# Performance work log

Measured on AMD Instinct MI355X. Metric: run time of the kernel, lower is better.

The kernel has to match this reference:

```python
import jax, jax.numpy as jnp
import numpy as np
import math

B, S, D = 2, 2048, 1024
H, KV, HD = 16, 4, 64
N_REP = H // KV
ROPE_THETA = 1.0e6


def _rope_tables(seq_len, head_dim, theta):
    inv_freq = 1.0 / (theta ** (np.arange(0, head_dim, 2, dtype=np.float32) / head_dim))
    t = np.arange(seq_len, dtype=np.float32)
    freqs = np.outer(t, inv_freq)                      # [S, HD/2]
    emb = np.concatenate([freqs, freqs], axis=-1)      # [S, HD]
    return jnp.asarray(np.cos(emb)), jnp.asarray(np.sin(emb))


def setup_inputs() -> dict:
    key = jax.random.key(0)
    ks = jax.random.split(key, 6)
    cos, sin = _rope_tables(S, HD, ROPE_THETA)
    scale = 0.02
    return {
        "x": jax.random.normal(ks[0], (B, S, D), dtype=jnp.float32),
        "cos": cos,
        "sin": sin,
        "Wq": jax.random.normal(ks[1], (D, H * HD), dtype=jnp.float32) * scale,
        "Wk": jax.random.normal(ks[2], (D, KV * HD), dtype=jnp.float32) * scale,
        "Wv": jax.random.normal(ks[3], (D, KV * HD), dtype=jnp.float32) * scale,
        "Wo": jax.random.normal(ks[4], (H * HD, D), dtype=jnp.float32) * scale,
    }


def _rotate_half(u):
    u1, u2 = u[..., : HD // 2], u[..., HD // 2 :]
    return jnp.concatenate([-u2, u1], axis=-1)


def reference(x, cos, sin, Wq, Wk, Wv, Wo):
    bsz, seq_len, _ = x.shape
    q = (x @ Wq).reshape(bsz, seq_len, H, HD)   # [B,S,H,HD]
    k = (x @ Wk).reshape(bsz, seq_len, KV, HD)  # [B,S,KV,HD]
    v = (x @ Wv).reshape(bsz, seq_len, KV, HD)

    # RoPE: cos/sin [S,HD] broadcast over batch and heads (unsqueeze_dim=1)
    c = cos[:seq_len][None, :, None, :]
    s = sin[:seq_len][None, :, None, :]
    q = q * c + _rotate_half(q) * s
    k = k * c + _rotate_half(k) * s

    # repeat_kv: expand KV heads groupwise to H heads
    k = jnp.repeat(k, N_REP, axis=2)  # [B,S,H,HD]
    v = jnp.repeat(v, N_REP, axis=2)

    q = q.transpose(0, 2, 1, 3)  # [B,H,S,HD]
    k = k.transpose(0, 2, 1, 3)
    v = v.transpose(0, 2, 1, 3)

    scores = jnp.einsum("bhqd,bhkd->bhqk", q, k) / math.sqrt(HD)
    causal = jnp.tril(jnp.ones((seq_len, seq_len), dtype=bool))
    scores = jnp.where(causal[None, None], scores, jnp.finfo(jnp.float32).min)
    probs = jax.nn.softmax(scores.astype(jnp.float32), axis=-1).astype(x.dtype)

    out = jnp.einsum("bhqk,bhkd->bhqd", probs, v)        # [B,H,S,HD]
    out = out.transpose(0, 2, 1, 3).reshape(bsz, seq_len, H * HD)
    return out @ Wo
```

## Files before the change

### kernel.cpp

```cpp
#include <hip/hip_runtime.h>

#define SS 2048
#define NH 16
#define NKV 4
#define HD 64

typedef __bf16 bf16;
typedef __bf16 bf16x8 __attribute__((ext_vector_type(8)));
typedef float f32x4 __attribute__((ext_vector_type(4)));

#define SM_SCALE 0.18033688011f

__device__ __forceinline__ void gl_lds16(const bf16* g, bf16* l) {
    __builtin_amdgcn_global_load_lds((const __attribute__((address_space(1))) void*)g,
                                     (__attribute__((address_space(3))) void*)l, 16, 0, 0);
}

__global__ __launch_bounds__(256) void prep_kernel(
    const float* __restrict__ Wq, const float* __restrict__ Wk,
    const float* __restrict__ Wv, const float* __restrict__ Wo,
    bf16* __restrict__ wqkv_t, bf16* __restrict__ wo_t)
{
    const int blk = blockIdx.x;
    const int tid = threadIdx.x;
    const float* W; bf16* Wt; int N, n0, k0;
    if (blk < 256)      { W = Wq; Wt = wqkv_t;                       N = 1024; n0 = (blk & 15) * 64;         k0 = (blk >> 4) * 64; }
    else if (blk < 320) { W = Wk; Wt = wqkv_t + (size_t)1024 * 1024; N = 256;  n0 = ((blk - 256) & 3) * 64;  k0 = ((blk - 256) >> 2) * 64; }
    else if (blk < 384) { W = Wv; Wt = wqkv_t + (size_t)1280 * 1024; N = 256;  n0 = ((blk - 320) & 3) * 64;  k0 = ((blk - 320) >> 2) * 64; }
    else                { W = Wo; Wt = wo_t;                         N = 1024; n0 = ((blk - 384) & 15) * 64; k0 = ((blk - 384) >> 4) * 64; }

    __shared__ float Ts[64][65];
    const int c = tid & 63, rr = tid >> 6;
    #pragma unroll
    for (int i = 0; i < 16; ++i) {
        const int kk = i * 4 + rr;
        Ts[kk][c] = W[(size_t)(k0 + kk) * N + n0 + c];
    }
    __syncthreads();
    #pragma unroll
    for (int i = 0; i < 16; ++i) {
        const int nn = i * 4 + rr;
        Wt[(size_t)(n0 + nn) * 1024 + k0 + c] = (bf16)Ts[c][nn];
    }
}

template<int EPI>
__global__ __launch_bounds__(256) void gemm_bt_kernel(
    const bf16* __restrict__ A, const float* __restrict__ Af,
    const bf16* __restrict__ Bt, float* __restrict__ C,
    const float* __restrict__ cosp, const float* __restrict__ sinp,
    bf16* __restrict__ qo, bf16* __restrict__ ko, bf16* __restrict__ vto,
    int M, int N, int K)
{
    __shared__ bf16 As[64 * 64];
    __shared__ bf16 Bs[128 * 64];
    const int m0 = blockIdx.x * 64, n0 = blockIdx.y * 128;
    const int tid = threadIdx.x;
    const int w = tid >> 6, lane = tid & 63, g = lane >> 4, li = lane & 15;
    const int wm = w >> 1, wn = w & 1;

    f32x4 acc[2][4];
    const f32x4 z = {0.f, 0.f, 0.f, 0.f};
    #pragma unroll
    for (int i = 0; i < 2; ++i)
        #pragma unroll
        for (int j = 0; j < 4; ++j) acc[i][j] = z;

    const int srow = tid >> 3;
    const int schunk = ((tid & 7) ^ (srow & 7)) * 8;
    const bf16* pB0 = Bt + (size_t)(n0 + srow) * K + schunk;
    const bf16* pB1 = Bt + (size_t)(n0 + 32 + srow) * K + schunk;
    const bf16* pB2 = Bt + (size_t)(n0 + 64 + srow) * K + schunk;
    const bf16* pB3 = Bt + (size_t)(n0 + 96 + srow) * K + schunk;
    bf16* lB0 = Bs + (size_t)w * 512;
    bf16* lB1 = Bs + 2048 + (size_t)w * 512;
    bf16* lB2 = Bs + 4096 + (size_t)w * 512;
    bf16* lB3 = Bs + 6144 + (size_t)w * 512;
    const bf16* pA0 = (EPI == 0) ? A + (size_t)(m0 + srow) * K + schunk : nullptr;
    const bf16* pA1 = (EPI == 0) ? A + (size_t)(m0 + 32 + srow) * K + schunk : nullptr;
    bf16* lA0 = As + (size_t)w * 512;
    bf16* lA1 = As + 2048 + (size_t)w * 512;

    for (int kk = 0; kk < K; kk += 64) {
        __syncthreads();
        if (EPI == 0) {
            gl_lds16(pA0 + kk, lA0);
            gl_lds16(pA1 + kk, lA1);
        } else {
            #pragma unroll
            for (int s = 0; s < 2; ++s) {
                const float* src = Af + (size_t)(m0 + s * 32 + srow) * K + kk + (tid & 7) * 8;
                const float4 v0 = *(const float4*)src;
                const float4 v1 = *(const float4*)(src + 4);
                bf16x8 t8;
                t8[0] = (bf16)v0.x; t8[1] = (bf16)v0.y; t8[2] = (bf16)v0.z; t8[3] = (bf16)v0.w;
                t8[4] = (bf16)v1.x; t8[5] = (bf16)v1.y; t8[6] = (bf16)v1.z; t8[7] = (bf16)v1.w;
                *(bf16x8*)&As[(s * 32 + srow) * 64 + schunk] = t8;
            }
        }
        gl_lds16(pB0 + kk, lB0);
        gl_lds16(pB1 + kk, lB1);
        gl_lds16(pB2 + kk, lB2);
        gl_lds16(pB3 + kk, lB3);
        __syncthreads();
        #pragma unroll
        for (int t = 0; t < 2; ++t) {
            const int phys = ((t * 4 + g) ^ (li & 7)) * 8;
            bf16x8 af[2], bfr[4];
            #pragma unroll
            for (int mi = 0; mi < 2; ++mi) af[mi] = *(const bf16x8*)&As[(wm * 32 + mi * 16 + li) * 64 + phys];
            #pragma unroll
            for (int ni = 0; ni < 4; ++ni) bfr[ni] = *(const bf16x8*)&Bs[(wn * 64 + ni * 16 + li) * 64 + phys];
            #pragma unroll
            for (int mi = 0; mi < 2; ++mi)
                #pragma unroll
                for (int ni = 0; ni < 4; ++ni)
                    acc[mi][ni] = __builtin_amdgcn_mfma_f32_16x16x32_bf16(af[mi], bfr[ni], acc[mi][ni], 0, 0, 0);
        }
    }

    const int row0 = m0 + wm * 32, col0 = n0 + wn * 64;
    if (EPI == 0) {
        #pragma unroll
        for (int mi = 0; mi < 2; ++mi)
            #pragma unroll
            for (int ni = 0; ni < 4; ++ni)
                #pragma unroll
                for (int r = 0; r < 4; ++r)
                    C[(size_t)(row0 + mi * 16 + g * 4 + r) * N + col0 + ni * 16 + li] = acc[mi][ni][r];
    } else {
        #pragma unroll
        for (int ni = 0; ni < 4; ++ni) {
            const int col = col0 + ni * 16 + li;
            const int d = col & 63;
            #pragma unroll
            for (int mi = 0; mi < 2; ++mi) {
                #pragma unroll
                for (int r = 0; r < 4; ++r) {
                    const int row = row0 + mi * 16 + g * 4 + r;
                    const int bb = row >> 11, s = row & 2047;
                    float val = acc[mi][ni][r];
                    if (col < 1280) {
                        const float pairv = acc[mi][ni ^ 2][r];
                        const float rot = (d < 32) ? -pairv : pairv;
                        val = val * cosp[s * 64 + d] + rot * sinp[s * 64 + d];
                    }
                    if (col < 1024) {
                        const int hh = col >> 6;
                        qo[(((size_t)bb * NH + hh) * SS + s) * HD + d] = (bf16)(val * SM_SCALE);
                    } else if (col < 1280) {
                        const int kh = (col - 1024) >> 6;
                        ko[(((size_t)bb * NKV + kh) * SS + s) * HD + d] = (bf16)val;
                    } else {
                        const int kh = (col - 1280) >> 6;
                        vto[(((size_t)bb * NKV + kh) * HD + d) * SS + s] = (bf16)val;
                    }
                }
            }
        }
    }
}

__global__ __launch_bounds__(256) void flash_kernel(const bf16* __restrict__ q, const bf16* __restrict__ k,
                                                    const bf16* __restrict__ vt, bf16* __restrict__ o)
{
    __shared__ bf16 Ks[128 * 64];
    __shared__ bf16 Vt[64 * 128];
    __shared__ bf16 Ps[4][16][72];

    const int blk = blockIdx.x;
    const int qt = 31 - (blk >> 5);
    const int h = blk & 15;
    const int b = (blk >> 4) & 1;
    const int kvh = h >> 2;
    const int tid = threadIdx.x;
    const int w = tid >> 6, lane = tid & 63, g = lane >> 4, li = lane & 15;

    const bf16* qh = q + ((size_t)b * NH + h) * SS * HD;
    const bf16* kh = k + ((size_t)b * NKV + kvh) * SS * HD;
    const bf16* vh = vt + ((size_t)b * NKV + kvh) * (size_t)HD * SS;

    bf16x8 ones;
    #pragma unroll
    for (int j = 0; j < 8; ++j) ones[j] = (bf16)1.0f;
    const f32x4 z = {0.f, 0.f, 0.f, 0.f};

    const bf16* qrow = qh + (size_t)(qt * 64 + w * 16 + li) * HD;
    bf16x8 qf[2];
    qf[0] = *(const bf16x8*)(qrow + g * 8);
    qf[1] = *(const bf16x8*)(qrow + 32 + g * 8);

    const int ksrow = tid >> 3;
    const int kchunk = ((tid & 7) ^ (ksrow & 7)) * 8;
    const int vsrow = tid >> 4;
    const int vchunk = (((tid & 15) ^ (vsrow & 7)) & 15) * 8;
    bf16* lK = Ks + (size_t)w * 512;
    bf16* lV = Vt + (size_t)w * 512;

    f32x4 o_acc[4], l_acc;
    #pragma unroll
    for (int nt = 0; nt < 4; ++nt) o_acc[nt] = z;
    l_acc = z;

    for (int kt0 = 0; kt0 <= qt; kt0 += 2) {
        __syncthreads();
        {
            #pragma unroll
            for (int s = 0; s < 4; ++s)
                gl_lds16(kh + (size_t)(kt0 * 64 + s * 32 + ksrow) * HD + kchunk, lK + s * 2048);
            #pragma unroll
            for (int s = 0; s < 4; ++s)
                gl_lds16(vh + (size_t)(s * 16 + vsrow) * SS + kt0 * 64 + vchunk, lV + s * 2048);
        }
        __syncthreads();

        #pragma unroll
        for (int sub = 0; sub < 2; ++sub) {
            const int kt = kt0 + sub;
            if (kt > qt) break;

            f32x4 s_acc[4];
            #pragma unroll
            for (int nt = 0; nt < 4; ++nt) s_acc[nt] = z;
            #pragma unroll
            for (int t = 0; t < 2; ++t)
                #pragma unroll
                for (int nt = 0; nt < 4; ++nt) {
                    const bf16x8 kf = *(const bf16x8*)&Ks[(sub * 64 + nt * 16 + li) * 64 + (((t * 4 + g) ^ (li & 7)) * 8)];
                    s_acc[nt] = __builtin_amdgcn_mfma_f32_16x16x32_bf16(qf[t], kf, s_acc[nt], 0, 0, 0);
                }

            if (kt == qt) {
                const int qr0 = qt * 64 + w * 16 + g * 4;
                #pragma unroll
                for (int nt = 0; nt < 4; ++nt) {
                    const int key = kt * 64 + nt * 16 + li;
                    #pragma unroll
                    for (int r = 0; r < 4; ++r) {
                        float sv = s_acc[nt][r];
                        if (key > qr0 + r) sv = -1e30f;
                        Ps[w][g * 4 + r][(nt * 16 + li) ^ (g * 16)] = (bf16)exp2f(sv);
                    }
                }
            } else {
                #pragma unroll
                for (int nt = 0; nt < 4; ++nt)
                    #pragma unroll
                    for (int r = 0; r < 4; ++r)
                        Ps[w][g * 4 + r][(nt * 16 + li) ^ (g * 16)] = (bf16)exp2f(s_acc[nt][r]);
            }

            #pragma unroll
            for (int t = 0; t < 2; ++t) {
                const bf16x8 pf = *(const bf16x8*)&Ps[w][li][(t * 32 + g * 8) ^ ((li >> 2) * 16)];
                l_acc = __builtin_amdgcn_mfma_f32_16x16x32_bf16(pf, ones, l_acc, 0, 0, 0);
                #pragma unroll
                for (int nt = 0; nt < 4; ++nt) {
                    const bf16x8 vf = *(const bf16x8*)&Vt[(nt * 16 + li) * 128 + (((sub * 8 + t * 4 + g) ^ (li & 7)) * 8)];
                    o_acc[nt] = __builtin_amdgcn_mfma_f32_16x16x32_bf16(pf, vf, o_acc[nt], 0, 0, 0);
                }
            }
        }
    }

    #pragma unroll
    for (int r = 0; r < 4; ++r) {
        const float inv = 1.f / l_acc[r];
        const int s = qt * 64 + w * 16 + g * 4 + r;
        bf16* orow = o + (((size_t)b * SS + s) * NH + h) * HD;
        #pragma unroll
        for (int nt = 0; nt < 4; ++nt) orow[nt * 16 + li] = (bf16)(o_acc[nt][r] * inv);
    }
}

extern "C" void kernel_launch(void* const* d_in, const int* in_sizes, int n_in,
                              void* d_out, int out_size, void* d_ws, size_t ws_size,
                              hipStream_t stream) {
    const float* x     = (const float*)d_in[0];
    const float* cos_t = (const float*)d_in[1];
    const float* sin_t = (const float*)d_in[2];
    const float* Wq    = (const float*)d_in[3];
    const float* Wk    = (const float*)d_in[4];
    const float* Wv    = (const float*)d_in[5];
    const float* Wo    = (const float*)d_in[6];
    float* out = (float*)d_out;

    char* wsb = (char*)d_ws;
    bf16* o_b    = (bf16*)(wsb);
    bf16* wqkv_t = (bf16*)(wsb + 8388608);
    bf16* wo_t   = (bf16*)(wsb + 11534336);
    bf16* q_b    = (bf16*)(wsb + 13631488);
    bf16* k_b    = (bf16*)(wsb + 22020096);
    bf16* vt_b   = (bf16*)(wsb + 24117248);

    prep_kernel<<<640, 256, 0, stream>>>(Wq, Wk, Wv, Wo, wqkv_t, wo_t);

    gemm_bt_kernel<2><<<dim3(64, 12), 256, 0, stream>>>(nullptr, x, wqkv_t, nullptr, cos_t, sin_t,
                                                        q_b, k_b, vt_b, 4096, 1536, 1024);
    flash_kernel<<<1024, 256, 0, stream>>>(q_b, k_b, vt_b, o_b);
    gemm_bt_kernel<0><<<dim3(64, 8), 256, 0, stream>>>(o_b, nullptr, wo_t, out, nullptr, nullptr,
                                                       nullptr, nullptr, nullptr, 4096, 1024, 1024);
}
```

Baseline: 166.7 us.

## Enlarge GEMM M-tile to 128 and transpose QK^T MFMA for vectorized P stores

Both GEMMs now use 128x128 output tiles instead of 64x128, with each wave computing 64x64 and the grid halved in the M dimension. This raises operand reuse per LDS load but cuts block count to 384 and 256, which may underfill the GPU's CUs. In the flash kernel, the QK^T MFMA operands are swapped so each lane holds four consecutive keys for one query row. P is then written to LDS as bf16x4 vectors in an XOR-swizzled layout, replacing scalar stores, and the causal mask indexing is adjusted to match.

```diff
diff --git a/kernel.cpp b/kernel.cpp
--- a/kernel.cpp
+++ b/kernel.cpp
@@ -6,6 +6,7 @@
 #define HD 64
 
 typedef __bf16 bf16;
+typedef __bf16 bf16x4 __attribute__((ext_vector_type(4)));
 typedef __bf16 bf16x8 __attribute__((ext_vector_type(8)));
 typedef float f32x4 __attribute__((ext_vector_type(4)));
 
@@ -52,43 +53,42 @@
     bf16* __restrict__ qo, bf16* __restrict__ ko, bf16* __restrict__ vto,
     int M, int N, int K)
 {
-    __shared__ bf16 As[64 * 64];
+    __shared__ bf16 As[128 * 64];
     __shared__ bf16 Bs[128 * 64];
-    const int m0 = blockIdx.x * 64, n0 = blockIdx.y * 128;
+    const int m0 = blockIdx.x * 128, n0 = blockIdx.y * 128;
     const int tid = threadIdx.x;
     const int w = tid >> 6, lane = tid & 63, g = lane >> 4, li = lane & 15;
     const int wm = w >> 1, wn = w & 1;
 
-    f32x4 acc[2][4];
+    f32x4 acc[4][4];
     const f32x4 z = {0.f, 0.f, 0.f, 0.f};
     #pragma unroll
-    for (int i = 0; i < 2; ++i)
+    for (int i = 0; i < 4; ++i)
         #pragma unroll
         for (int j = 0; j < 4; ++j) acc[i][j] = z;
 
     const int srow = tid >> 3;
     const int schunk = ((tid & 7) ^ (srow & 7)) * 8;
-    const bf16* pB0 = Bt + (size_t)(n0 + srow) * K + schunk;
-    const bf16* pB1 = Bt + (size_t)(n0 + 32 + srow) * K + schunk;
-    const bf16* pB2 = Bt + (size_t)(n0 + 64 + srow) * K + schunk;
-    const bf16* pB3 = Bt + (size_t)(n0 + 96 + srow) * K + schunk;
-    bf16* lB0 = Bs + (size_t)w * 512;
-    bf16* lB1 = Bs + 2048 + (size_t)w * 512;
-    bf16* lB2 = Bs + 4096 + (size_t)w * 512;
-    bf16* lB3 = Bs + 6144 + (size_t)w * 512;
-    const bf16* pA0 = (EPI == 0) ? A + (size_t)(m0 + srow) * K + schunk : nullptr;
-    const bf16* pA1 = (EPI == 0) ? A + (size_t)(m0 + 32 + srow) * K + schunk : nullptr;
-    bf16* lA0 = As + (size_t)w * 512;
-    bf16* lA1 = As + 2048 + (size_t)w * 512;
+    const bf16* pB[4];
+    const bf16* pA[4];
+    bf16* lB[4];
+    bf16* lA[4];
+    #pragma unroll
+    for (int s = 0; s < 4; ++s) {
+        pB[s] = Bt + (size_t)(n0 + s * 32 + srow) * K + schunk;
+        lB[s] = Bs + s * 2048 + (size_t)w * 512;
+        if (EPI == 0) pA[s] = A + (size_t)(m0 + s * 32 + srow) * K + schunk;
+        lA[s] = As + s * 2048 + (size_t)w * 512;
+    }
 
     for (int kk = 0; kk < K; kk += 64) {
         __syncthreads();
         if (EPI == 0) {
-            gl_lds16(pA0 + kk, lA0);
-            gl_lds16(pA1 + kk, lA1);
+            #pragma unroll
+            for (int s = 0; s < 4; ++s) gl_lds16(pA[s] + kk, lA[s]);
         } else {
             #pragma unroll
-            for (int s = 0; s < 2; ++s) {
+            for (int s = 0; s < 4; ++s) {
                 const float* src = Af + (size_t)(m0 + s * 32 + srow) * K + kk + (tid & 7) * 8;
                 const float4 v0 = *(const float4*)src;
                 const float4 v1 = *(const float4*)(src + 4);
@@ -98,31 +98,29 @@
                 *(bf16x8*)&As[(s * 32 + srow) * 64 + schunk] = t8;
             }
         }
-        gl_lds16(pB0 + kk, lB0);
-        gl_lds16(pB1 + kk, lB1);
-        gl_lds16(pB2 + kk, lB2);
-        gl_lds16(pB3 + kk, lB3);
+        #pragma unroll
+        for (int s = 0; s < 4; ++s) gl_lds16(pB[s] + kk, lB[s]);
         __syncthreads();
         #pragma unroll
         for (int t = 0; t < 2; ++t) {
             const int phys = ((t * 4 + g) ^ (li & 7)) * 8;
-            bf16x8 af[2], bfr[4];
-            #pragma unroll
-            for (int mi = 0; mi < 2; ++mi) af[mi] = *(const bf16x8*)&As[(wm * 32 + mi * 16 + li) * 64 + phys];
+            bf16x8 af[4], bfr[4];
+            #pragma unroll
+            for (int mi = 0; mi < 4; ++mi) af[mi] = *(const bf16x8*)&As[(wm * 64 + mi * 16 + li) * 64 + phys];
             #pragma unroll
             for (int ni = 0; ni < 4; ++ni) bfr[ni] = *(const bf16x8*)&Bs[(wn * 64 + ni * 16 + li) * 64 + phys];
             #pragma unroll
-            for (int mi = 0; mi < 2; ++mi)
+            for (int mi = 0; mi < 4; ++mi)
                 #pragma unroll
                 for (int ni = 0; ni < 4; ++ni)
                     acc[mi][ni] = __builtin_amdgcn_mfma_f32_16x16x32_bf16(af[mi], bfr[ni], acc[mi][ni], 0, 0, 0);
         }
     }
 
-    const int row0 = m0 + wm * 32, col0 = n0 + wn * 64;
+    const int row0 = m0 + wm * 64, col0 = n0 + wn * 64;
     if (EPI == 0) {
         #pragma unroll
-        for (int mi = 0; mi < 2; ++mi)
+        for (int mi = 0; mi < 4; ++mi)
             #pragma unroll
             for (int ni = 0; ni < 4; ++ni)
                 #pragma unroll
@@ -134,7 +132,7 @@
             const int col = col0 + ni * 16 + li;
             const int d = col & 63;
             #pragma unroll
-            for (int mi = 0; mi < 2; ++mi) {
+            for (int mi = 0; mi < 4; ++mi) {
                 #pragma unroll
                 for (int r = 0; r < 4; ++r) {
                     const int row = row0 + mi * 16 + g * 4 + r;
@@ -166,7 +164,7 @@
 {
     __shared__ bf16 Ks[128 * 64];
     __shared__ bf16 Vt[64 * 128];
-    __shared__ bf16 Ps[4][16][72];
+    __shared__ bf16 Ps[4][16 * 64];
 
     const int blk = blockIdx.x;
     const int qt = 31 - (blk >> 5);
@@ -197,6 +195,8 @@
     bf16* lK = Ks + (size_t)w * 512;
     bf16* lV = Vt + (size_t)w * 512;
 
+    const int xm = (li & 7) << 1;
+
     f32x4 o_acc[4], l_acc;
     #pragma unroll
     for (int nt = 0; nt < 4; ++nt) o_acc[nt] = z;
@@ -227,32 +227,35 @@
                 #pragma unroll
                 for (int nt = 0; nt < 4; ++nt) {
                     const bf16x8 kf = *(const bf16x8*)&Ks[(sub * 64 + nt * 16 + li) * 64 + (((t * 4 + g) ^ (li & 7)) * 8)];
-                    s_acc[nt] = __builtin_amdgcn_mfma_f32_16x16x32_bf16(qf[t], kf, s_acc[nt], 0, 0, 0);
+                    s_acc[nt] = __builtin_amdgcn_mfma_f32_16x16x32_bf16(kf, qf[t], s_acc[nt], 0, 0, 0);
                 }
 
             if (kt == qt) {
-                const int qr0 = qt * 64 + w * 16 + g * 4;
+                const int qrow_in = w * 16 + li;
                 #pragma unroll
                 for (int nt = 0; nt < 4; ++nt) {
-                    const int key = kt * 64 + nt * 16 + li;
+                    bf16x4 p4;
                     #pragma unroll
                     for (int r = 0; r < 4; ++r) {
                         float sv = s_acc[nt][r];
-                        if (key > qr0 + r) sv = -1e30f;
-                        Ps[w][g * 4 + r][(nt * 16 + li) ^ (g * 16)] = (bf16)exp2f(sv);
+                        if (nt * 16 + g * 4 + r > qrow_in) sv = -1e30f;
+                        p4[r] = (bf16)exp2f(sv);
                     }
+                    *(bf16x4*)&Ps[w][li * 64 + (((nt * 4 + g) ^ xm) * 4)] = p4;
                 }
             } else {
                 #pragma unroll
-                for (int nt = 0; nt < 4; ++nt)
+                for (int nt = 0; nt < 4; ++nt) {
+                    bf16x4 p4;
                     #pragma unroll
-                    for (int r = 0; r < 4; ++r)
-                        Ps[w][g * 4 + r][(nt * 16 + li) ^ (g * 16)] = (bf16)exp2f(s_acc[nt][r]);
+                    for (int r = 0; r < 4; ++r) p4[r] = (bf16)exp2f(s_acc[nt][r]);
+                    *(bf16x4*)&Ps[w][li * 64 + (((nt * 4 + g) ^ xm) * 4)] = p4;
+                }
             }
 
             #pragma unroll
             for (int t = 0; t < 2; ++t) {
-                const bf16x8 pf = *(const bf16x8*)&Ps[w][li][(t * 32 + g * 8) ^ ((li >> 2) * 16)];
+                const bf16x8 pf = *(const bf16x8*)&Ps[w][li * 64 + (((t * 8 + g * 2) ^ xm) * 4)];
                 l_acc = __builtin_amdgcn_mfma_f32_16x16x32_bf16(pf, ones, l_acc, 0, 0, 0);
                 #pragma unroll
                 for (int nt = 0; nt < 4; ++nt) {
@@ -295,9 +298,9 @@
 
     prep_kernel<<<640, 256, 0, stream>>>(Wq, Wk, Wv, Wo, wqkv_t, wo_t);
 
-    gemm_bt_kernel<2><<<dim3(64, 12), 256, 0, stream>>>(nullptr, x, wqkv_t, nullptr, cos_t, sin_t,
+    gemm_bt_kernel<2><<<dim3(32, 12), 256, 0, stream>>>(nullptr, x, wqkv_t, nullptr, cos_t, sin_t,
                                                         q_b, k_b, vt_b, 4096, 1536, 1024);
     flash_kernel<<<1024, 256, 0, stream>>>(q_b, k_b, vt_b, o_b);
-    gemm_bt_kernel<0><<<dim3(64, 8), 256, 0, stream>>>(o_b, nullptr, wo_t, out, nullptr, nullptr,
+    gemm_bt_kernel<0><<<dim3(32, 8), 256, 0, stream>>>(o_b, nullptr, wo_t, out, nullptr, nullptr,
                                                        nullptr, nullptr, nullptr, 4096, 1024, 1024);
 }
```

New measurement: 184.1 us. 10.5% more time.
